# Kernel tuning notes

Measured on AMD Instinct MI355X. Metric: run time of the kernel, lower is better.

The kernel has to match this reference:

```python
import jax, jax.numpy as jnp
import numpy as np

T, B, V = 50, 128, 8000          # seq_len, batch, inputDimSize
A = 728                          # numAncestors
NEMB = V + A                     # rows of W_emb
E, H, ATT, C, L = 128, 128, 100, 283, 5


def setup_inputs() -> dict:
    key = jax.random.key(0)
    ks = jax.random.split(key, 12)
    x = jax.random.normal(ks[0], (T, B, V), jnp.float32)
    mask = jnp.ones((T, B), jnp.float32)
    leaves = jax.random.randint(ks[1], (V, L), 0, NEMB)
    ancestors = jax.random.randint(ks[2], (V, L), 0, NEMB)
    W_emb = jax.random.uniform(ks[3], (NEMB, E), jnp.float32)
    W_attention = jax.random.uniform(ks[4], (2 * E, ATT), jnp.float32)
    b_attention = jnp.zeros((ATT,), jnp.float32)
    v_attention = jax.random.uniform(ks[5], (ATT,), jnp.float32)
    gru_w_ih = jax.random.normal(ks[6], (3 * H, E), jnp.float32) * 0.1
    gru_w_hh = jax.random.normal(ks[7], (3 * H, H), jnp.float32) * 0.1
    gru_b_ih = jnp.zeros((3 * H,), jnp.float32)
    gru_b_hh = jnp.zeros((3 * H,), jnp.float32)
    W_output = jax.random.uniform(ks[8], (H, C), jnp.float32) * 0.1
    b_output = jnp.zeros((C,), jnp.float32)
    return {"x": x, "mask": mask, "W_emb": W_emb,
            "W_attention": W_attention, "b_attention": b_attention,
            "v_attention": v_attention, "gru_w_ih": gru_w_ih,
            "gru_w_hh": gru_w_hh, "gru_b_ih": gru_b_ih,
            "gru_b_hh": gru_b_hh, "W_output": W_output,
            "b_output": b_output, "leaves": leaves, "ancestors": ancestors}


def reference(x, mask, W_emb, W_attention, b_attention, v_attention,
              gru_w_ih, gru_w_hh, gru_b_ih, gru_b_hh,
              W_output, b_output, leaves, ancestors):
    # --- Attention over ontology ancestors (gather + MLP + softmax + reduce) ---
    le = W_emb[leaves]       # [V, L, E]
    an = W_emb[ancestors]    # [V, L, E]
    att_in = jnp.concatenate([le, an], axis=-1)              # [V, L, 2E]
    mlp = jnp.tanh(att_in @ W_attention + b_attention)       # [V, L, ATT]
    pre = mlp @ v_attention                                  # [V, L]
    att = jax.nn.softmax(pre, axis=1)                        # softmax over ancestors
    emb = jnp.einsum('vle,vl->ve', an, att)                  # [V, E]

    # --- project multi-hot visits into embedding space ---
    x_emb = jnp.tanh(jnp.einsum('tbv,ve->tbe', x, emb))      # [T, B, E]

    # --- torch-style single-layer GRU via scan (time-major) ---
    def cell(h, xt):
        gx = xt @ gru_w_ih.T + gru_b_ih                      # [B, 3H]
        gh = h @ gru_w_hh.T + gru_b_hh
        xr, xz, xn = jnp.split(gx, 3, axis=-1)
        hr, hz, hn = jnp.split(gh, 3, axis=-1)
        r = jax.nn.sigmoid(xr + hr)
        z = jax.nn.sigmoid(xz + hz)
        n = jnp.tanh(xn + r * hn)
        h_new = (1.0 - z) * n + z * h
        return h_new, h_new

    h0 = jnp.zeros((B, H), x_emb.dtype)
    _, hidden = jax.lax.scan(cell, h0, x_emb)                # [T, B, H]

    # dropout_rate = 0 -> identity
    # exp / sum == softmax over the class dim
    out = jax.nn.softmax(hidden @ W_output + b_output, axis=2)  # [T, B, C]
    return out * mask[:, :, None]
```

## Files before the change

kernel.cpp:

```cpp
#include <hip/hip_runtime.h>


typedef unsigned short u16;
typedef unsigned int   u32;
typedef short bf16x8 __attribute__((ext_vector_type(8)));
typedef float f32x4  __attribute__((ext_vector_type(4)));

typedef __attribute__((address_space(1))) u32 gas_u32;
typedef __attribute__((address_space(3))) u32 las_u32;

union U4 { u32 u[4]; bf16x8 v; uint4 q; };

__device__ __forceinline__ float uaf(u32 u){ union{u32 u; float f;} c; c.u=u; return c.f; }
__device__ __forceinline__ u32 fau(float f){ union{u32 u; float f;} c; c.f=f; return c.u; }
__device__ __forceinline__ u16 f2bf(float f){ u32 u=fau(f); return (u16)((u + 0x7fffu + ((u>>16)&1u))>>16); }
__device__ __forceinline__ float sigm(float x){ return 1.f/(1.f+__expf(-x)); }

__device__ __forceinline__ void gll16(const void* g, void* l){
    __builtin_amdgcn_global_load_lds((const gas_u32*)g, (las_u32*)l, 16, 0, 0);
}

__device__ __forceinline__ void split8(const float* f, bf16x8* hi, bf16x8* lo){
    U4 H, L;
    #pragma unroll
    for (int j=0;j<4;++j){
        float f0=f[2*j], f1=f[2*j+1];
        u32 u0=fau(f0), u1=fau(f1);
        u32 t0=u0+0x7fffu+((u0>>16)&1u);
        u32 t1=u1+0x7fffu+((u1>>16)&1u);
        u32 h1=t1&0xffff0000u;
        H.u[j]=(t0>>16)|h1;
        float l0=f0-uaf(t0&0xffff0000u);
        float l1=f1-uaf(h1);
        u32 v0=fau(l0), v1=fau(l1);
        u32 s0=v0+0x7fffu+((v0>>16)&1u);
        u32 s1=v1+0x7fffu+((v1>>16)&1u);
        L.u[j]=(s0>>16)|(s1&0xffff0000u);
    }
    *hi=H.v; *lo=L.v;
}

__device__ __forceinline__ void split1(float f, u16& h, u16& l){
    u32 u=fau(f); u32 t=u+0x7fffu+((u>>16)&1u); h=(u16)(t>>16);
    float lf=f-uaf(t&0xffff0000u); l=f2bf(lf);
}

#define MFMA(a,b,c) __builtin_amdgcn_mfma_f32_16x16x32_bf16(a,b,c,0,0,0)

__global__ __launch_bounds__(256,1) void prep_watt_kernel(
    const float* __restrict__ W_att, u16* __restrict__ WT_h, u16* __restrict__ WT_l)
{
    int n=blockIdx.x, k=threadIdx.x;
    float f = (n<100)? W_att[k*100+n] : 0.f;
    u16 h,l; split1(f,h,l);
    WT_h[n*256+k]=h; WT_l[n*256+k]=l;
}

__global__ __launch_bounds__(256,1) void prep_whh_kernel(
    const float* __restrict__ whh, u32* __restrict__ out)
{
    int i=blockIdx.x*256+threadIdx.x;
    int j=i>>6, p=i&63;
    u32 a=(u32)f2bf(whh[j*128+2*p]);
    u32 b=(u32)f2bf(whh[j*128+2*p+1]);
    out[i]=a|(b<<16);
}

__global__ __launch_bounds__(256,1) void transpose_wih_kernel(
    const float* __restrict__ w_ih, float* __restrict__ w_ihT)
{
    int i=blockIdx.x*256+threadIdx.x;
    int e=i/384, j=i-e*384;
    w_ihT[i]=w_ih[j*128+e];
}

__global__ __launch_bounds__(256,1) void attn_mlp_kernel(
    const float* __restrict__ W_emb, const float* __restrict__ b_att,
    const float* __restrict__ v_att, const int* __restrict__ leaves,
    const int* __restrict__ anc, const u16* __restrict__ WT_h,
    const u16* __restrict__ WT_l, float* __restrict__ emb_f)
{
    __shared__ __align__(16) char smem[61440];
    short* Ah=(short*)smem;
    short* Al=(short*)(smem+16384);
    short* Bh=(short*)(smem+32768);
    short* Bl=(short*)(smem+47104);
    float* mlp_s=(float*)smem;
    __shared__ float s_pre[128];
    __shared__ float s_vatt[112];
    __shared__ float s_attw[128];
    __shared__ int   s_leaf[128], s_anc[128];

    const int tid=threadIdx.x;
    const int wave=tid>>6, lane=tid&63;
    const int vb5=blockIdx.x*125;

    if (tid<125){ s_leaf[tid]=leaves[vb5+tid]; s_anc[tid]=anc[vb5+tid]; }
    else if (tid<128){ s_leaf[tid]=leaves[vb5]; s_anc[tid]=anc[vb5]; }
    if (tid<100) s_vatt[tid]=v_att[tid];

    f32x4 acc[2][7];
    const f32x4 zf={0.f,0.f,0.f,0.f};
    #pragma unroll
    for (int mi=0;mi<2;++mi)
        #pragma unroll
        for (int ni=0;ni<7;++ni) acc[mi][ni]=zf;

    const int fr=lane&15, fq=lane>>4;

    for (int kc=0;kc<4;++kc){
        __syncthreads();
        {
            int r=tid>>1, seg=tid&1;
            int src=(kc<2)? s_leaf[r] : s_anc[r];
            const float* srcp = W_emb + (size_t)src*128 + (kc&1)*64 + seg*32;
            float buf[32];
            #pragma unroll
            for (int i=0;i<8;++i) *(f32x4*)(buf+4*i) = *(const f32x4*)(srcp+4*i);
            #pragma unroll
            for (int j=0;j<4;++j){
                bf16x8 hv, lv; split8(buf+8*j, &hv, &lv);
                U4 H,L; H.v=hv; L.v=lv;
                *(uint4*)&Ah[r*64+seg*32+j*8] = H.q;
                *(uint4*)&Al[r*64+seg*32+j*8] = L.q;
            }
        }
        for (int c=wave;c<14;c+=4){
            size_t go=(size_t)(c*8+(lane>>3))*512 + (size_t)kc*128 + (size_t)(lane&7)*16;
            gll16((const char*)WT_h+go, Bh+c*512);
            gll16((const char*)WT_l+go, Bl+c*512);
        }
        __syncthreads();

        #pragma unroll
        for (int ks=0;ks<2;++ks){
            bf16x8 ah[2],al[2],bh[7],bl[7];
            #pragma unroll
            for (int mi=0;mi<2;++mi){
                int row=wave*32+mi*16+fr;
                ah[mi]=*(const bf16x8*)&Ah[row*64+ks*32+fq*8];
                al[mi]=*(const bf16x8*)&Al[row*64+ks*32+fq*8];
            }
            #pragma unroll
            for (int ni=0;ni<7;++ni){
                int rowb=ni*16+fr;
                bh[ni]=*(const bf16x8*)&Bh[rowb*64+ks*32+fq*8];
                bl[ni]=*(const bf16x8*)&Bl[rowb*64+ks*32+fq*8];
            }
            #pragma unroll
            for (int mi=0;mi<2;++mi)
                #pragma unroll
                for (int ni=0;ni<7;++ni){
                    acc[mi][ni]=MFMA(ah[mi],bh[ni],acc[mi][ni]);
                    acc[mi][ni]=MFMA(ah[mi],bl[ni],acc[mi][ni]);
                    acc[mi][ni]=MFMA(al[mi],bh[ni],acc[mi][ni]);
                }
        }
    }
    __syncthreads();
    #pragma unroll
    for (int ni=0;ni<7;++ni){
        int col=ni*16+fr;
        float bb=(col<100)? b_att[col] : 0.f;
        #pragma unroll
        for (int mi=0;mi<2;++mi){
            int rb=wave*32+mi*16+fq*4;
            #pragma unroll
            for (int r=0;r<4;++r)
                mlp_s[(rb+r)*112+col]=tanhf(acc[mi][ni][r]+bb);
        }
    }
    __syncthreads();
    if (tid<128){
        float s=0.f;
        for (int n=0;n<100;++n) s+=mlp_s[tid*112+n]*s_vatt[n];
        s_pre[tid]=s;
    }
    __syncthreads();
    if (tid<25){
        float p[5], mx=-1e30f;
        #pragma unroll
        for (int l=0;l<5;++l){ p[l]=s_pre[tid*5+l]; mx=fmaxf(mx,p[l]); }
        float s=0.f;
        #pragma unroll
        for (int l=0;l<5;++l){ p[l]=__expf(p[l]-mx); s+=p[l]; }
        float inv=1.f/s;
        #pragma unroll
        for (int l=0;l<5;++l) s_attw[tid*5+l]=p[l]*inv;
    }
    __syncthreads();
    for (int o=tid;o<3200;o+=256){
        int v=o>>7, e=o&127;
        float s=0.f;
        #pragma unroll
        for (int l=0;l<5;++l)
            s += s_attw[v*5+l]*W_emb[(size_t)s_anc[v*5+l]*128+e];
        emb_f[(size_t)(blockIdx.x*25+v)*128+e]=s;
    }
}

__global__ __launch_bounds__(256,1) void emb_split_kernel(
    const float* __restrict__ emb_f, u16* __restrict__ hiT, u16* __restrict__ loT)
{
    __shared__ float tile[64*128];
    const int tid=threadIdx.x;
    const int vb=blockIdx.x*64;
    for (int i=tid;i<2048;i+=256){
        int row=i>>5, q=i&31;
        *(f32x4*)&tile[row*128+q*4] = *(const f32x4*)&emb_f[(size_t)(vb+row)*128+q*4];
    }
    __syncthreads();
    u32* hw=(u32*)hiT; u32* lw=(u32*)loT;
    for (int o=tid;o<4096;o+=256){
        int e=o>>5, p=o&31;
        float f0=tile[(2*p)*128+e], f1=tile[(2*p+1)*128+e];
        u16 h0,l0,h1,l1; split1(f0,h0,l0); split1(f1,h1,l1);
        size_t base=(size_t)e*4000 + (size_t)(vb>>1) + p;
        hw[base]=(u32)h0|((u32)h1<<16);
        lw[base]=(u32)l0|((u32)l1<<16);
    }
}

__global__ __launch_bounds__(256,4) void gemm_xemb_kernel(
    const float* __restrict__ x, const u16* __restrict__ bhT, const u16* __restrict__ blT,
    float* __restrict__ partials)
{
    __shared__ __align__(16) float Asf[32*64];
    __shared__ __align__(16) short Bh[128*64];
    __shared__ __align__(16) short Bl[128*64];

    const int tid=threadIdx.x, wave=tid>>6, lane=tid&63;
    const int mt=blockIdx.x%200, ks=blockIdx.x/200;
    const int mbase=mt*32;
    const int k0=ks*1600;

    f32x4 acc[2][2];
    const f32x4 zf={0.f,0.f,0.f,0.f};
    #pragma unroll
    for (int i=0;i<2;++i)
        #pragma unroll
        for (int j=0;j<2;++j) acc[i][j]=zf;

    const char* xb=(const char*)x;
    const char* bhb=(const char*)bhT;
    const char* blb=(const char*)blT;
    const int fr=lane&15, fq=lane>>4;
    const int nbase=wave*32;

    const int ar = lane>>4;
    const int ac0 = lane&15;
    const int br = lane>>3;
    const int bc0 = lane&7;

    for (int kk=k0; kk<k0+1600; kk+=64){
        __syncthreads();
        #pragma unroll
        for (int ii=0;ii<2;++ii){
            int t=wave*2+ii;
            int r=t*4+ar;
            int c=ac0^(r&15);
            gll16(xb + ((size_t)(mbase+r)*8000 + kk + c*4)*4,
                  (char*)Asf + (size_t)t*1024);
        }
        #pragma unroll
        for (int ii=0;ii<4;++ii){
            int s=wave*4+ii;
            int r=s*8+br;
            int c=bc0^(r&7);
            size_t go=((size_t)r*8000 + kk + c*8)*2;
            gll16(bhb+go, (char*)Bh + (size_t)s*1024);
            gll16(blb+go, (char*)Bl + (size_t)s*1024);
        }
        __syncthreads();

        #pragma unroll
        for (int kh=0;kh<2;++kh){
            bf16x8 ah[2],al[2],bh[2],bl[2];
            #pragma unroll
            for (int mi=0;mi<2;++mi){
                int row=mi*16+fr;
                int c0=kh*8+fq*2;
                float buf[8];
                *(f32x4*)&buf[0]=*(const f32x4*)&Asf[(row*16+((c0  )^(row&15)))*4];
                *(f32x4*)&buf[4]=*(const f32x4*)&Asf[(row*16+((c0+1)^(row&15)))*4];
                split8(buf,&ah[mi],&al[mi]);
            }
            #pragma unroll
            for (int ni=0;ni<2;++ni){
                int rowb=nbase+ni*16+fr;
                int ch=rowb*8+((kh*4+fq)^(rowb&7));
                bh[ni]=*(const bf16x8*)&Bh[ch*8];
                bl[ni]=*(const bf16x8*)&Bl[ch*8];
            }
            #pragma unroll
            for (int mi=0;mi<2;++mi)
                #pragma unroll
                for (int ni=0;ni<2;++ni){
                    acc[mi][ni]=MFMA(ah[mi],bh[ni],acc[mi][ni]);
                    acc[mi][ni]=MFMA(ah[mi],bl[ni],acc[mi][ni]);
                    acc[mi][ni]=MFMA(al[mi],bh[ni],acc[mi][ni]);
                }
        }
    }

    float* pout=partials + ((size_t)ks*6400+mbase)*128;
    #pragma unroll
    for (int mi=0;mi<2;++mi)
        #pragma unroll
        for (int ni=0;ni<2;++ni)
            #pragma unroll
            for (int r=0;r<4;++r)
                pout[(size_t)(mi*16+fq*4+r)*128 + nbase+ni*16+fr]=acc[mi][ni][r];
}

__global__ __launch_bounds__(128,1) void sumtanh_gx_kernel(
    const float* __restrict__ partials, const float* __restrict__ w_ihT,
    const float* __restrict__ b_ih, float* __restrict__ GX)
{
    __shared__ float sx[2048];
    const int tid=threadIdx.x;
    const int rb=blockIdx.x*16;
    for (int i=tid;i<2048;i+=128){
        size_t o=(size_t)rb*128+i;
        float s=0.f;
        #pragma unroll
        for (int k=0;k<5;++k) s+=partials[(size_t)k*819200+o];
        sx[i]=tanhf(s);
    }
    __syncthreads();

    float acc0[16],acc1[16],acc2[16];
    #pragma unroll
    for (int r=0;r<16;++r){ acc0[r]=0.f; acc1[r]=0.f; acc2[r]=0.f; }
    for (int e=0;e<128;++e){
        float w0=w_ihT[e*384+tid];
        float w1=w_ihT[e*384+tid+128];
        float w2=w_ihT[e*384+tid+256];
        #pragma unroll
        for (int r=0;r<16;++r){
            float xv=sx[r*128+e];
            acc0[r]=fmaf(xv,w0,acc0[r]);
            acc1[r]=fmaf(xv,w1,acc1[r]);
            acc2[r]=fmaf(xv,w2,acc2[r]);
        }
    }
    float b0=b_ih[tid], b1=b_ih[tid+128], b2=b_ih[tid+256];
    #pragma unroll
    for (int r=0;r<16;++r){
        float* gp=GX+(size_t)(rb+r)*384;
        gp[tid]=acc0[r]+b0;
        gp[tid+128]=acc1[r]+b1;
        gp[tid+256]=acc2[r]+b2;
    }
}

__global__ __launch_bounds__(384,1) void gru_scan_kernel(
    const u32* __restrict__ whh_p, const float* __restrict__ b_hh,
    const float* __restrict__ GX, float* __restrict__ hidden)
{
    __shared__ __align__(16) u16 shb[128];
    __shared__ float sgh[384];
    const int tid=threadIdx.x, b=blockIdx.x;

    float wf[128];
    #pragma unroll
    for (int q=0;q<64;++q){
        u32 u=whh_p[tid*64+q];
        wf[2*q]  =uaf(u<<16);
        wf[2*q+1]=uaf(u&0xffff0000u);
    }
    float hreg=0.f;
    if (tid<128) shb[tid]=0;
    const float bb=b_hh[tid];
    __syncthreads();

    for (int t=0;t<50;++t){
        float gx0=0.f,gx1=0.f,gx2=0.f;
        if (tid<128){
            const float* gp=GX+((size_t)t*128+b)*384;
            gx0=gp[tid]; gx1=gp[128+tid]; gx2=gp[256+tid];
        }
        float acc=0.f;
        #pragma unroll
        for (int p=0;p<16;++p){
            U4 c; c.v=*(const bf16x8*)&shb[p*8];
            #pragma unroll
            for (int j=0;j<4;++j){
                u32 u=c.u[j];
                acc=fmaf(uaf(u<<16),         wf[p*8+2*j],   acc);
                acc=fmaf(uaf(u&0xffff0000u), wf[p*8+2*j+1], acc);
            }
        }
        sgh[tid]=acc+bb;
        __syncthreads();
        if (tid<128){
            float r=sigm(gx0+sgh[tid]);
            float z=sigm(gx1+sgh[128+tid]);
            float n=tanhf(gx2+r*sgh[256+tid]);
            float hn=(1.f-z)*n+z*hreg;
            hreg=hn;
            hidden[((size_t)t*128+b)*128+tid]=hn;
            shb[tid]=f2bf(hn);
        }
        __syncthreads();
    }
}

__global__ __launch_bounds__(128,1) void logits_softmax_kernel(
    const float* __restrict__ hidden, const float* __restrict__ W_out,
    const float* __restrict__ b_out, const float* __restrict__ mask,
    float* __restrict__ out)
{
    __shared__ float shd[2048];
    __shared__ float slog[16*288];
    const int tid=threadIdx.x;
    const int rb=blockIdx.x*16;
    for (int i=tid;i<2048;i+=128) shd[i]=hidden[(size_t)rb*128+i];
    __syncthreads();

    const int c0=tid, c1=tid+128, c2=tid+256;
    const bool v2=(c2<283);
    float acc0[16],acc1[16],acc2[16];
    #pragma unroll
    for (int r=0;r<16;++r){ acc0[r]=0.f; acc1[r]=0.f; acc2[r]=0.f; }
    for (int h=0;h<128;++h){
        const float* wr=W_out+h*283;
        float w0=wr[c0];
        float w1=wr[c1];
        float w2=v2? wr[c2] : 0.f;
        #pragma unroll
        for (int r=0;r<16;++r){
            float hv=shd[r*128+h];
            acc0[r]=fmaf(hv,w0,acc0[r]);
            acc1[r]=fmaf(hv,w1,acc1[r]);
            acc2[r]=fmaf(hv,w2,acc2[r]);
        }
    }
    float b0=b_out[c0], b1=b_out[c1], b2v=v2? b_out[c2] : 0.f;
    #pragma unroll
    for (int r=0;r<16;++r){
        slog[r*288+c0]=acc0[r]+b0;
        slog[r*288+c1]=acc1[r]+b1;
        if (v2) slog[r*288+c2]=acc2[r]+b2v;
    }
    __syncthreads();

    const int wv=tid>>6, lane=tid&63;
    #pragma unroll
    for (int rr=0;rr<8;++rr){
        int r=wv*8+rr;
        int m=rb+r;
        float v[5];
        float mx=-1e30f;
        #pragma unroll
        for (int i=0;i<5;++i){
            int c=lane+i*64;
            v[i]=(c<283)? slog[r*288+c] : -1e30f;
            mx=fmaxf(mx,v[i]);
        }
        #pragma unroll
        for (int off=32;off>0;off>>=1) mx=fmaxf(mx,__shfl_xor(mx,off,64));
        float s=0.f;
        #pragma unroll
        for (int i=0;i<5;++i){
            int c=lane+i*64;
            v[i]=(c<283)? __expf(v[i]-mx) : 0.f;
            s+=v[i];
        }
        #pragma unroll
        for (int off=32;off>0;off>>=1) s+=__shfl_xor(s,off,64);
        const float sc=mask[m]/s;
        float* op=out+(size_t)m*283;
        #pragma unroll
        for (int i=0;i<5;++i){
            int c=lane+i*64;
            if (c<283) op[c]=v[i]*sc;
        }
    }
}

extern "C" void kernel_launch(void* const* d_in, const int* in_sizes, int n_in,
                              void* d_out, int out_size, void* d_ws, size_t ws_size,
                              hipStream_t stream) {
    const float* x      = (const float*)d_in[0];
    const float* mask   = (const float*)d_in[1];
    const float* W_emb  = (const float*)d_in[2];
    const float* W_att  = (const float*)d_in[3];
    const float* b_att  = (const float*)d_in[4];
    const float* v_att  = (const float*)d_in[5];
    const float* w_ih   = (const float*)d_in[6];
    const float* w_hh   = (const float*)d_in[7];
    const float* b_ih   = (const float*)d_in[8];
    const float* b_hh   = (const float*)d_in[9];
    const float* W_out  = (const float*)d_in[10];
    const float* b_out  = (const float*)d_in[11];
    const int* leaves   = (const int*)d_in[12];
    const int* anc      = (const int*)d_in[13];
    float* out = (float*)d_out;

    char* w = (char*)d_ws;
    u16*   WT_h    = (u16*)(w + 0);
    u16*   WT_l    = (u16*)(w + 57344);
    u32*   whh_p   = (u32*)(w + 114688);
    float* w_ihT   = (float*)(w + 212992);
    u16*   emb_hiT = (u16*)(w + 409600);
    u16*   emb_loT = (u16*)(w + 2457600);
    float* emb_f   = (float*)(w + 4505600);
    float* partials= (float*)(w + 8601600);
    float* GX      = (float*)(w + 24985600);
    float* hidden  = (float*)(w + 34816000);

    prep_watt_kernel<<<112, 256, 0, stream>>>(W_att, WT_h, WT_l);
    prep_whh_kernel<<<96, 256, 0, stream>>>(w_hh, whh_p);
    transpose_wih_kernel<<<192, 256, 0, stream>>>(w_ih, w_ihT);
    attn_mlp_kernel<<<320, 256, 0, stream>>>(W_emb, b_att, v_att, leaves, anc,
                                             WT_h, WT_l, emb_f);
    emb_split_kernel<<<125, 256, 0, stream>>>(emb_f, emb_hiT, emb_loT);
    gemm_xemb_kernel<<<1000, 256, 0, stream>>>(x, emb_hiT, emb_loT, partials);
    sumtanh_gx_kernel<<<400, 128, 0, stream>>>(partials, w_ihT, b_ih, GX);
    gru_scan_kernel<<<128, 384, 0, stream>>>(whh_p, b_hh, GX, hidden);
    logits_softmax_kernel<<<400, 128, 0, stream>>>(hidden, W_out, b_out, mask, out);
}
```

Measured before the change: 523.7 us.

## Presplit A tile into bf16 in LDS, prefetch GX, widen GX and logits blocks

The x-embedding GEMM now loads x into registers one k-step ahead and splits it into bf16 hi/lo once when storing to LDS. This replaces the direct global-to-LDS fp32 copy and removes the per-fragment split from the MFMA loop. The GRU scan prefetches the next step's input gates to hide global latency on the serial path. The GX projection and logits kernels use one output column per thread with wider blocks (384 and 320 threads), which cuts per-thread registers and raises parallelism. The trade-off is more register staging in the GEMM and idle waves during the logits softmax phase.

Measured after the change: 474.2 us. 1.1x faster.

```diff
diff --git a/kernel.cpp b/kernel.cpp
--- a/kernel.cpp
+++ b/kernel.cpp
@@ -225,7 +225,8 @@
     const float* __restrict__ x, const u16* __restrict__ bhT, const u16* __restrict__ blT,
     float* __restrict__ partials)
 {
-    __shared__ __align__(16) float Asf[32*64];
+    __shared__ __align__(16) short Ah[32*64];
+    __shared__ __align__(16) short Al[32*64];
     __shared__ __align__(16) short Bh[128*64];
     __shared__ __align__(16) short Bl[128*64];
 
@@ -241,26 +242,28 @@
         #pragma unroll
         for (int j=0;j<2;++j) acc[i][j]=zf;
 
-    const char* xb=(const char*)x;
     const char* bhb=(const char*)bhT;
     const char* blb=(const char*)blT;
     const int fr=lane&15, fq=lane>>4;
     const int nbase=wave*32;
 
-    const int ar = lane>>4;
-    const int ac0 = lane&15;
-    const int br = lane>>3;
-    const int bc0 = lane&7;
+    const int sr=tid>>3, sc=tid&7;
+    const float* agp = x + (size_t)(mbase+sr)*8000 + k0 + sc*8;
+    bf16x8* awh = (bf16x8*)&Ah[sr*64 + ((sc^(sr&7))<<3)];
+    bf16x8* awl = (bf16x8*)&Al[sr*64 + ((sc^(sr&7))<<3)];
+
+    const int br=lane>>3, bc0=lane&7;
+
+    f32x4 pa0 = *(const f32x4*)agp;
+    f32x4 pa1 = *(const f32x4*)(agp+4);
 
     for (int kk=k0; kk<k0+1600; kk+=64){
         __syncthreads();
-        #pragma unroll
-        for (int ii=0;ii<2;++ii){
-            int t=wave*2+ii;
-            int r=t*4+ar;
-            int c=ac0^(r&15);
-            gll16(xb + ((size_t)(mbase+r)*8000 + kk + c*4)*4,
-                  (char*)Asf + (size_t)t*1024);
+        {
+            float buf[8];
+            *(f32x4*)&buf[0]=pa0; *(f32x4*)&buf[4]=pa1;
+            bf16x8 hv,lv; split8(buf,&hv,&lv);
+            *awh=hv; *awl=lv;
         }
         #pragma unroll
         for (int ii=0;ii<4;++ii){
@@ -273,17 +276,20 @@
         }
         __syncthreads();
 
+        if (kk+64 < k0+1600){
+            const float* ag = agp + (kk + 64 - k0);
+            pa0=*(const f32x4*)ag; pa1=*(const f32x4*)(ag+4);
+        }
+
         #pragma unroll
         for (int kh=0;kh<2;++kh){
             bf16x8 ah[2],al[2],bh[2],bl[2];
             #pragma unroll
             for (int mi=0;mi<2;++mi){
                 int row=mi*16+fr;
-                int c0=kh*8+fq*2;
-                float buf[8];
-                *(f32x4*)&buf[0]=*(const f32x4*)&Asf[(row*16+((c0  )^(row&15)))*4];
-                *(f32x4*)&buf[4]=*(const f32x4*)&Asf[(row*16+((c0+1)^(row&15)))*4];
-                split8(buf,&ah[mi],&al[mi]);
+                int ci=(kh*4+fq)^(row&7);
+                ah[mi]=*(const bf16x8*)&Ah[row*64+ci*8];
+                al[mi]=*(const bf16x8*)&Al[row*64+ci*8];
             }
             #pragma unroll
             for (int ni=0;ni<2;++ni){
@@ -313,14 +319,14 @@
                 pout[(size_t)(mi*16+fq*4+r)*128 + nbase+ni*16+fr]=acc[mi][ni][r];
 }
 
-__global__ __launch_bounds__(128,1) void sumtanh_gx_kernel(
+__global__ __launch_bounds__(384,2) void sumtanh_gx_kernel(
     const float* __restrict__ partials, const float* __restrict__ w_ihT,
     const float* __restrict__ b_ih, float* __restrict__ GX)
 {
     __shared__ float sx[2048];
     const int tid=threadIdx.x;
     const int rb=blockIdx.x*16;
-    for (int i=tid;i<2048;i+=128){
+    for (int i=tid;i<2048;i+=384){
         size_t o=(size_t)rb*128+i;
         float s=0.f;
         #pragma unroll
@@ -329,29 +335,18 @@
     }
     __syncthreads();
 
-    float acc0[16],acc1[16],acc2[16];
-    #pragma unroll
-    for (int r=0;r<16;++r){ acc0[r]=0.f; acc1[r]=0.f; acc2[r]=0.f; }
+    float acc[16];
+    #pragma unroll
+    for (int r=0;r<16;++r) acc[r]=0.f;
     for (int e=0;e<128;++e){
         float w0=w_ihT[e*384+tid];
-        float w1=w_ihT[e*384+tid+128];
-        float w2=w_ihT[e*384+tid+256];
-        #pragma unroll
-        for (int r=0;r<16;++r){
-            float xv=sx[r*128+e];
-            acc0[r]=fmaf(xv,w0,acc0[r]);
-            acc1[r]=fmaf(xv,w1,acc1[r]);
-            acc2[r]=fmaf(xv,w2,acc2[r]);
-        }
-    }
-    float b0=b_ih[tid], b1=b_ih[tid+128], b2=b_ih[tid+256];
-    #pragma unroll
-    for (int r=0;r<16;++r){
-        float* gp=GX+(size_t)(rb+r)*384;
-        gp[tid]=acc0[r]+b0;
-        gp[tid+128]=acc1[r]+b1;
-        gp[tid+256]=acc2[r]+b2;
-    }
+        #pragma unroll
+        for (int r=0;r<16;++r) acc[r]=fmaf(sx[r*128+e],w0,acc[r]);
+    }
+    float b0=b_ih[tid];
+    #pragma unroll
+    for (int r=0;r<16;++r)
+        GX[(size_t)(rb+r)*384+tid]=acc[r]+b0;
 }
 
 __global__ __launch_bounds__(384,1) void gru_scan_kernel(
@@ -372,13 +367,19 @@
     float hreg=0.f;
     if (tid<128) shb[tid]=0;
     const float bb=b_hh[tid];
+
+    float gx0=0.f,gx1=0.f,gx2=0.f;
+    if (tid<128){
+        const float* gp=GX+(size_t)b*384;
+        gx0=gp[tid]; gx1=gp[128+tid]; gx2=gp[256+tid];
+    }
     __syncthreads();
 
     for (int t=0;t<50;++t){
-        float gx0=0.f,gx1=0.f,gx2=0.f;
-        if (tid<128){
-            const float* gp=GX+((size_t)t*128+b)*384;
-            gx0=gp[tid]; gx1=gp[128+tid]; gx2=gp[256+tid];
+        float nx0=0.f,nx1=0.f,nx2=0.f;
+        if (tid<128 && t<49){
+            const float* gp=GX+((size_t)(t+1)*128+b)*384;
+            nx0=gp[tid]; nx1=gp[128+tid]; nx2=gp[256+tid];
         }
         float acc=0.f;
         #pragma unroll
@@ -403,10 +404,11 @@
             shb[tid]=f2bf(hn);
         }
         __syncthreads();
-    }
-}
-
-__global__ __launch_bounds__(128,1) void logits_softmax_kernel(
+        gx0=nx0; gx1=nx1; gx2=nx2;
+    }
+}
+
+__global__ __launch_bounds__(320,2) void logits_softmax_kernel(
     const float* __restrict__ hidden, const float* __restrict__ W_out,
     const float* __restrict__ b_out, const float* __restrict__ mask,
     float* __restrict__ out)
@@ -415,66 +417,58 @@
     __shared__ float slog[16*288];
     const int tid=threadIdx.x;
     const int rb=blockIdx.x*16;
-    for (int i=tid;i<2048;i+=128) shd[i]=hidden[(size_t)rb*128+i];
-    __syncthreads();
-
-    const int c0=tid, c1=tid+128, c2=tid+256;
-    const bool v2=(c2<283);
-    float acc0[16],acc1[16],acc2[16];
-    #pragma unroll
-    for (int r=0;r<16;++r){ acc0[r]=0.f; acc1[r]=0.f; acc2[r]=0.f; }
+    for (int i=tid;i<2048;i+=320) shd[i]=hidden[(size_t)rb*128+i];
+    __syncthreads();
+
+    const bool act=(tid<283);
+    const int cl=act? tid : 282;
+    float acc[16];
+    #pragma unroll
+    for (int r=0;r<16;++r) acc[r]=0.f;
     for (int h=0;h<128;++h){
-        const float* wr=W_out+h*283;
-        float w0=wr[c0];
-        float w1=wr[c1];
-        float w2=v2? wr[c2] : 0.f;
-        #pragma unroll
-        for (int r=0;r<16;++r){
-            float hv=shd[r*128+h];
-            acc0[r]=fmaf(hv,w0,acc0[r]);
-            acc1[r]=fmaf(hv,w1,acc1[r]);
-            acc2[r]=fmaf(hv,w2,acc2[r]);
-        }
-    }
-    float b0=b_out[c0], b1=b_out[c1], b2v=v2? b_out[c2] : 0.f;
-    #pragma unroll
-    for (int r=0;r<16;++r){
-        slog[r*288+c0]=acc0[r]+b0;
-        slog[r*288+c1]=acc1[r]+b1;
-        if (v2) slog[r*288+c2]=acc2[r]+b2v;
+        float w0=W_out[h*283+cl];
+        #pragma unroll
+        for (int r=0;r<16;++r) acc[r]=fmaf(shd[r*128+h],w0,acc[r]);
+    }
+    float b0=b_out[cl];
+    if (act){
+        #pragma unroll
+        for (int r=0;r<16;++r) slog[r*288+tid]=acc[r]+b0;
     }
     __syncthreads();
 
     const int wv=tid>>6, lane=tid&63;
-    #pragma unroll
-    for (int rr=0;rr<8;++rr){
-        int r=wv*8+rr;
-        int m=rb+r;
-        float v[5];
-        float mx=-1e30f;
-        #pragma unroll
-        for (int i=0;i<5;++i){
-            int c=lane+i*64;
-            v[i]=(c<283)? slog[r*288+c] : -1e30f;
-            mx=fmaxf(mx,v[i]);
-        }
-        #pragma unroll
-        for (int off=32;off>0;off>>=1) mx=fmaxf(mx,__shfl_xor(mx,off,64));
-        float s=0.f;
-        #pragma unroll
-        for (int i=0;i<5;++i){
-            int c=lane+i*64;
-            v[i]=(c<283)? __expf(v[i]-mx) : 0.f;
-            s+=v[i];
-        }
-        #pragma unroll
-        for (int off=32;off>0;off>>=1) s+=__shfl_xor(s,off,64);
-        const float sc=mask[m]/s;
-        float* op=out+(size_t)m*283;
-        #pragma unroll
-        for (int i=0;i<5;++i){
-            int c=lane+i*64;
-            if (c<283) op[c]=v[i]*sc;
+    if (wv<4){
+        #pragma unroll
+        for (int rr=0;rr<4;++rr){
+            int r=wv*4+rr;
+            int m=rb+r;
+            float v[5];
+            float mx=-1e30f;
+            #pragma unroll
+            for (int i=0;i<5;++i){
+                int c=lane+i*64;
+                v[i]=(c<283)? slog[r*288+c] : -1e30f;
+                mx=fmaxf(mx,v[i]);
+            }
+            #pragma unroll
+            for (int off=32;off>0;off>>=1) mx=fmaxf(mx,__shfl_xor(mx,off,64));
+            float s=0.f;
+            #pragma unroll
+            for (int i=0;i<5;++i){
+                int c=lane+i*64;
+                v[i]=(c<283)? __expf(v[i]-mx) : 0.f;
+                s+=v[i];
+            }
+            #pragma unroll
+            for (int off=32;off>0;off>>=1) s+=__shfl_xor(s,off,64);
+            const float sc=mask[m]/s;
+            float* op=out+(size_t)m*283;
+            #pragma unroll
+            for (int i=0;i<5;++i){
+                int c=lane+i*64;
+                if (c<283) op[c]=v[i]*sc;
+            }
         }
     }
 }
@@ -517,7 +511,7 @@
                                              WT_h, WT_l, emb_f);
     emb_split_kernel<<<125, 256, 0, stream>>>(emb_f, emb_hiT, emb_loT);
     gemm_xemb_kernel<<<1000, 256, 0, stream>>>(x, emb_hiT, emb_loT, partials);
-    sumtanh_gx_kernel<<<400, 128, 0, stream>>>(partials, w_ihT, b_ih, GX);
+    sumtanh_gx_kernel<<<400, 384, 0, stream>>>(partials, w_ihT, b_ih, GX);
     gru_scan_kernel<<<128, 384, 0, stream>>>(whh_p, b_hh, GX, hidden);
-    logits_softmax_kernel<<<400, 128, 0, stream>>>(hidden, W_out, b_out, mask, out);
-}
+    logits_softmax_kernel<<<400, 320, 0, stream>>>(hidden, W_out, b_out, mask, out);
+}
```
